# Optimization experiments

Measured on AMD Instinct MI355X. Metric: run time of the kernel, lower is better.

The kernel has to match this reference:

```python
import jax, jax.numpy as jnp
import numpy as np

B, N, D = 4, 4096, 64   # batch, num points, point-feature channels
K = 24                  # original_k_neighbors
GO = 128                # graph_out_channel = max(32, (D*2//8)*8)
MLP = [64, 128, 256]
HALF = MLP[-1] // 2     # graph_feature_mapping out channels
EPS = 1e-5

def leaky(x):
    return jnp.where(x > 0, x, 0.2 * x)

def bn(x, gamma, beta, axes):
    # training-mode batch norm (biased variance, like torch normalization); channel last
    m = jnp.mean(x, axes, keepdims=True)
    v = jnp.var(x, axes, keepdims=True)
    return (x - m) * jax.lax.rsqrt(v + EPS) * gamma + beta

def knn_idx(p, k):
    # p: [B,N,3] -> indices of k nearest neighbors (self excluded), [B,N,k]
    sq = jnp.sum(p * p, -1)
    dist = sq[:, :, None] + sq[:, None, :] - 2.0 * jnp.einsum('bnc,bmc->bnm', p, p)
    _, idx = jax.lax.top_k(-dist, k + 1)   # smallest k+1 distances
    return idx[:, :, 1:]

def setup_inputs():
    key = jax.random.key(0)
    ks = jax.random.split(key, 8)
    w = lambda i, s: jax.random.normal(ks[i], s, jnp.float32) * 0.05
    return {
        'xyz': jax.random.normal(ks[0], (B, 3, N), jnp.float32),
        'points': jax.random.normal(ks[1], (B, D, N), jnp.float32),
        'ec_w': w(2, (GO, 2 * D)),
        'ec_g': jnp.ones((GO,), jnp.float32), 'ec_b': jnp.zeros((GO,), jnp.float32),
        'gm_w': w(3, (HALF, GO)),
        'gm_g': jnp.ones((HALF,), jnp.float32), 'gm_b': jnp.zeros((HALF,), jnp.float32),
        'w0': w(4, (MLP[0], D + 3)), 'bias0': jnp.zeros((MLP[0],), jnp.float32),
        'g0': jnp.ones((MLP[0],), jnp.float32), 'be0': jnp.zeros((MLP[0],), jnp.float32),
        'w1': w(5, (MLP[1], MLP[0])), 'bias1': jnp.zeros((MLP[1],), jnp.float32),
        'g1': jnp.ones((MLP[1],), jnp.float32), 'be1': jnp.zeros((MLP[1],), jnp.float32),
        'w2': w(6, (MLP[2], MLP[1])), 'bias2': jnp.zeros((MLP[2],), jnp.float32),
        'g2': jnp.ones((MLP[2],), jnp.float32), 'be2': jnp.zeros((MLP[2],), jnp.float32),
        'fu_w': w(7, (MLP[2], MLP[2] + HALF)),
        'fu_g': jnp.ones((MLP[2],), jnp.float32), 'fu_b': jnp.zeros((MLP[2],), jnp.float32),
    }

def reference(xyz, points, ec_w, ec_g, ec_b, gm_w, gm_g, gm_b,
              w0, bias0, g0, be0, w1, bias1, g1, be1, w2, bias2, g2, be2,
              fu_w, fu_g, fu_b):
    xyz_t = jnp.transpose(xyz, (0, 2, 1))     # [B,N,3]
    pts_t = jnp.transpose(points, (0, 2, 1))  # [B,N,D]
    edges = knn_idx(xyz_t, K)                 # [B,N,K]
    # --- EdgeConv on original graph ---
    nb = jax.vmap(lambda f, e: f[e])(pts_t, edges)  # gather: [B,N,K,D]
    ctr = pts_t[:, :, None, :]
    ef = jnp.concatenate([jnp.broadcast_to(ctr, nb.shape), nb - ctr], -1)  # [B,N,K,2D]
    h = jnp.einsum('bnkc,oc->bnko', ef, ec_w)
    h = leaky(bn(h, ec_g, ec_b, (0, 1, 2)))
    gfeat = jnp.max(h, axis=2)                # max over neighbors -> [B,N,GO]
    # --- graph_feature_mapping ---
    gm = jnp.einsum('bnc,oc->bno', gfeat, gm_w)
    gm = leaky(bn(gm, gm_g, gm_b, (0, 1)))    # [B,N,HALF]
    # --- group_all PointNet MLP ---
    g = jnp.concatenate([xyz_t, pts_t], -1)   # [B,N,D+3]
    for wl, bl, gl, bel in ((w0, bias0, g0, be0), (w1, bias1, g1, be1), (w2, bias2, g2, be2)):
        g = jax.nn.relu(bn(jnp.einsum('bnc,oc->bno', g, wl) + bl, gl, bel, (0, 1)))
    point_feat = jnp.max(g, axis=1)           # [B, MLP[-1]]
    graph_glob = jnp.max(gm, axis=1)          # [B, HALF]
    # --- fusion ---
    fused = jnp.concatenate([point_feat, graph_glob], -1)
    f = jnp.einsum('bc,oc->bo', fused, fu_w)
    f = leaky(bn(f, fu_g, fu_b, (0,)))
    return f[:, :, None]                      # [B, MLP[-1], 1]
```

## Files before the change

### kernel.cpp

```cpp
#include <hip/hip_runtime.h>

#define NPTS 4096
#define QN   16384
#define KNN  24

static constexpr size_t OFF_EDGES = 0;
static constexpr size_t OFF_BIG   = 393216;
static constexpr size_t OFF_A     = OFF_BIG;
static constexpr size_t OFF_C     = OFF_BIG + 2097152;
static constexpr size_t OFF_M     = OFF_BIG + 4194304;
static constexpr size_t OFF_GM    = OFF_BIG + 6553600;
static constexpr size_t OFF_L0    = OFF_GM + 2097152;
static constexpr size_t OFF_L1    = OFF_L0 + 1048576;
static constexpr size_t OFF_L2    = OFF_L1 + 2097152;
static constexpr size_t ST_BASE   = OFF_L2 + 4194304;
static constexpr size_t ST_BN1    = ST_BASE;
static constexpr size_t ST_GM     = ST_BASE + 256;
static constexpr size_t ST_L0     = ST_BASE + 512;
static constexpr size_t ST_L1     = ST_BASE + 640;
static constexpr size_t ST_L2     = ST_BASE + 896;
static constexpr size_t OFF_PF    = ST_BASE + 1408;
static constexpr size_t OFF_GG    = ST_BASE + 2432;
static constexpr size_t ST_COUNT  = 2944;

__device__ inline unsigned fmap(float f) {
    unsigned u = __float_as_uint(f);
    return (u & 0x80000000u) ? ~u : (u | 0x80000000u);
}
__device__ inline float funmap(unsigned u) {
    unsigned v = (u & 0x80000000u) ? (u & 0x7fffffffu) : ~u;
    return __uint_as_float(v);
}

__device__ inline void xcd_map(int bid, int& b, int& chunk) {
    b = (bid & 7) >> 1;
    chunk = ((bid >> 3) << 1) | (bid & 1);
}

__global__ __launch_bounds__(256) void knn_kernel(const float* __restrict__ xyz,
                                                  int* __restrict__ edges) {
    __shared__ float4 cand[1024];
    __shared__ unsigned long long buf[4][128];
    int b = blockIdx.y;
    int wave = threadIdx.x >> 6;
    int lane = threadIdx.x & 63;
    int n = blockIdx.x * 4 + wave;
    const float* xb = xyz + (size_t)b * 3 * 4096;
    unsigned long long* wbuf = buf[wave];

    float xq = xb[n], yq = xb[4096 + n], zq = xb[8192 + n];
    float sqq = __fadd_rn(__fadd_rn(__fmul_rn(xq, xq), __fmul_rn(yq, yq)), __fmul_rn(zq, zq));

    unsigned T = 0xFFFFFFFFu;
    int count = 0;

    auto reduce = [&]() {
        unsigned long long ka = (lane < count) ? wbuf[lane] : ~0ull;
        int ra = 0;
        if (count > 64) {
            unsigned long long kb = (lane + 64 < count) ? wbuf[lane + 64] : ~0ull;
            int rb = 0;
            for (int j = 0; j < count; ++j) {
                unsigned long long kj = wbuf[j];
                ra += (kj < ka);
                rb += (kj < kb);
            }
            if (rb < 25) wbuf[rb] = kb;
        } else {
            for (int j = 0; j < count; ++j) {
                unsigned long long kj = wbuf[j];
                ra += (kj < ka);
            }
        }
        if (ra < 25) wbuf[ra] = ka;
        count = 25;
        T = (unsigned)(wbuf[24] >> 32);
    };

    for (int strip = 0; strip < 4; ++strip) {
        __syncthreads();
        for (int i = threadIdx.x; i < 1024; i += 256) {
            int j = strip * 1024 + i;
            float x = xb[j], y = xb[4096 + j], z = xb[8192 + j];
            float sq = __fadd_rn(__fadd_rn(__fmul_rn(x, x), __fmul_rn(y, y)), __fmul_rn(z, z));
            cand[i] = make_float4(x, y, z, sq);
        }
        __syncthreads();

        for (int t = 0; t < 16; ++t) {
            float4 cv = cand[t * 64 + lane];
            float dot = __fadd_rn(__fadd_rn(__fmul_rn(xq, cv.x), __fmul_rn(yq, cv.y)), __fmul_rn(zq, cv.z));
            float d = __fsub_rn(__fadd_rn(sqq, cv.w), __fmul_rn(2.0f, dot));
            unsigned du = fmap(d);
            bool surv = (du <= T);
            unsigned long long m = __ballot(surv);
            if (m) {
                if (surv) {
                    int ofs = __popcll(m & ((1ull << lane) - 1ull));
                    unsigned idx = (unsigned)(strip * 1024 + t * 64 + lane);
                    wbuf[count + ofs] = ((unsigned long long)du << 32) | idx;
                }
                count += (int)__popcll(m);
                if (count >= 64) reduce();
            }
        }
    }
    reduce();
    if (lane >= 1 && lane < 25)
        edges[((size_t)(b * 4096 + n)) * KNN + lane - 1] = (int)(unsigned)(wbuf[lane] & 0xFFFFFFFFull);
}

__global__ __launch_bounds__(256) void feat_kernel(const float* __restrict__ pts,
                                                   const float* __restrict__ ec_w,
                                                   float* __restrict__ afeat,
                                                   float* __restrict__ cfeat) {
    __shared__ float inl[64 * 65];
    __shared__ float wa[64 * 132];
    __shared__ float wc[64 * 132];
    int b, chunk;
    xcd_map(blockIdx.x, b, chunk);
    int n0 = chunk * 64;

    for (int idx = threadIdx.x; idx < 64 * 64; idx += 256) {
        int c = idx >> 6, p = idx & 63;
        inl[p * 65 + c] = pts[((size_t)(b * 64 + c) << 12) + n0 + p];
    }
    for (int idx = threadIdx.x; idx < 128 * 64; idx += 256) {
        int o = idx >> 6, cc = idx & 63;
        float w1 = ec_w[o * 128 + cc], w2 = ec_w[o * 128 + 64 + cc];
        wa[cc * 132 + o] = w1 - w2;
        wc[cc * 132 + o] = w2;
    }
    __syncthreads();

    int ng = threadIdx.x & 15, og = threadIdx.x >> 4;
    float acca[4][8], accc[4][8];
    #pragma unroll
    for (int r = 0; r < 4; ++r)
        #pragma unroll
        for (int i = 0; i < 8; ++i) { acca[r][i] = 0.f; accc[r][i] = 0.f; }

    for (int c = 0; c < 64; ++c) {
        float pv[4];
        #pragma unroll
        for (int r = 0; r < 4; ++r) pv[r] = inl[(ng * 4 + r) * 65 + c];
        const float* wra = &wa[c * 132 + og * 8];
        const float* wrc = &wc[c * 132 + og * 8];
        float4 a0 = *(const float4*)&wra[0];
        float4 a1 = *(const float4*)&wra[4];
        float4 c0 = *(const float4*)&wrc[0];
        float4 c1 = *(const float4*)&wrc[4];
        float wva[8] = {a0.x, a0.y, a0.z, a0.w, a1.x, a1.y, a1.z, a1.w};
        float wvc[8] = {c0.x, c0.y, c0.z, c0.w, c1.x, c1.y, c1.z, c1.w};
        #pragma unroll
        for (int r = 0; r < 4; ++r)
            #pragma unroll
            for (int i = 0; i < 8; ++i) {
                acca[r][i] = fmaf(pv[r], wva[i], acca[r][i]);
                accc[r][i] = fmaf(pv[r], wvc[i], accc[r][i]);
            }
    }
    __syncthreads();
    float* outl = wa;
    size_t base = (((size_t)b << 12) + n0) * 128;

    #pragma unroll
    for (int r = 0; r < 4; ++r)
        #pragma unroll
        for (int i = 0; i < 8; ++i)
            outl[(ng * 4 + r) * 132 + og * 8 + i] = acca[r][i];
    __syncthreads();
    for (int idx = threadIdx.x; idx < 64 * 128; idx += 256) {
        int p = idx >> 7, o = idx & 127;
        afeat[base + idx] = outl[p * 132 + o];
    }
    __syncthreads();
    #pragma unroll
    for (int r = 0; r < 4; ++r)
        #pragma unroll
        for (int i = 0; i < 8; ++i)
            outl[(ng * 4 + r) * 132 + og * 8 + i] = accc[r][i];
    __syncthreads();
    for (int idx = threadIdx.x; idx < 64 * 128; idx += 256) {
        int p = idx >> 7, o = idx & 127;
        cfeat[base + idx] = outl[p * 132 + o];
    }
}

__global__ __launch_bounds__(256) void gather_stats_kernel(const float* __restrict__ afeat,
                                                           const float* __restrict__ cfeat,
                                                           const int* __restrict__ edges,
                                                           float* __restrict__ M,
                                                           float* __restrict__ st) {
    __shared__ int eL[16 * KNN];
    __shared__ float red[8][132];
    int b, chunk;
    xcd_map(blockIdx.x, b, chunk);
    int q0 = b * 4096 + chunk * 16;
    for (int idx = threadIdx.x; idx < 16 * KNN; idx += 256) eL[idx] = edges[(size_t)q0 * KNN + idx];
    __syncthreads();

    int m = threadIdx.x & 31;
    int g = threadIdx.x >> 5;
    int bbase = b << 12;
    float s1[4] = {0.f, 0.f, 0.f, 0.f}, s2[4] = {0.f, 0.f, 0.f, 0.f};

    #pragma unroll
    for (int half = 0; half < 2; ++half) {
        int p = g + half * 8;
        int q = q0 + p;
        float mx0 = -__builtin_inff(), mx1 = mx0, mx2 = mx0, mx3 = mx0;
        float sv0 = 0.f, sv1 = 0.f, sv2 = 0.f, sv3 = 0.f;
        float qv0 = 0.f, qv1 = 0.f, qv2 = 0.f, qv3 = 0.f;
        #pragma unroll 8
        for (int k = 0; k < KNN; ++k) {
            int e = eL[p * KNN + k];
            float4 v = *(const float4*)&cfeat[((size_t)(bbase + e) << 7) + m * 4];
            mx0 = fmaxf(mx0, v.x); sv0 += v.x; qv0 = fmaf(v.x, v.x, qv0);
            mx1 = fmaxf(mx1, v.y); sv1 += v.y; qv1 = fmaf(v.y, v.y, qv1);
            mx2 = fmaxf(mx2, v.z); sv2 += v.z; qv2 = fmaf(v.z, v.z, qv2);
            mx3 = fmaxf(mx3, v.w); sv3 += v.w; qv3 = fmaf(v.w, v.w, qv3);
        }
        float4 a = *(const float4*)&afeat[((size_t)q << 7) + m * 4];
        float4 mo = make_float4(a.x + mx0, a.y + mx1, a.z + mx2, a.w + mx3);
        *(float4*)&M[((size_t)q << 7) + m * 4] = mo;
        s1[0] += fmaf(24.f, a.x, sv0); s2[0] += 24.f * a.x * a.x + 2.f * a.x * sv0 + qv0;
        s1[1] += fmaf(24.f, a.y, sv1); s2[1] += 24.f * a.y * a.y + 2.f * a.y * sv1 + qv1;
        s1[2] += fmaf(24.f, a.z, sv2); s2[2] += 24.f * a.z * a.z + 2.f * a.z * sv2 + qv2;
        s1[3] += fmaf(24.f, a.w, sv3); s2[3] += 24.f * a.w * a.w + 2.f * a.w * sv3 + qv3;
    }
    #pragma unroll
    for (int j = 0; j < 4; ++j) red[g][m * 4 + j] = s1[j];
    __syncthreads();
    if (threadIdx.x < 128) {
        float t = 0.f;
        #pragma unroll
        for (int gg = 0; gg < 8; ++gg) t += red[gg][threadIdx.x];
        atomicAdd(&st[threadIdx.x], t);
    }
    __syncthreads();
    #pragma unroll
    for (int j = 0; j < 4; ++j) red[g][m * 4 + j] = s2[j];
    __syncthreads();
    if (threadIdx.x < 128) {
        float t = 0.f;
        #pragma unroll
        for (int gg = 0; gg < 8; ++gg) t += red[gg][threadIdx.x];
        atomicAdd(&st[128 + threadIdx.x], t);
    }
}

template<int I, int O, int OSPLIT, int MODE>
__global__ __launch_bounds__(256) void layer_kernel(
    const float* __restrict__ inraw, const float* __restrict__ inst, float rcnt,
    const float* __restrict__ ing, const float* __restrict__ inbe,
    const float* __restrict__ W, const float* __restrict__ bias,
    const float* __restrict__ xyz, const float* __restrict__ pts,
    float* __restrict__ outraw, float* __restrict__ outst)
{
    constexpr int OH = O / OSPLIT;
    constexpr int IP = (I & 1) ? I : I + 1;
    constexpr int OP = OH + 4;
    constexpr int OW = OH / 16;
    __shared__ float inl[64 * IP];
    __shared__ float wl[64 * OP];
    __shared__ float ns[I], nb[I];

    int b, chunk;
    xcd_map(blockIdx.x, b, chunk);
    int q0 = b * 4096 + chunk * 64;
    int o0 = blockIdx.y * OH;

    if (MODE != 0) {
        if (threadIdx.x < I) {
            int c = threadIdx.x;
            float m = inst[c] * rcnt;
            float v = inst[I + c] * rcnt - m * m;
            float inv = 1.0f / sqrtf(v + 1e-5f);
            float sc = inv * ing[c];
            ns[c] = sc;
            nb[c] = inbe[c] - m * sc;
        }
        __syncthreads();
        const float* src = inraw + (size_t)q0 * I;
        for (int idx = threadIdx.x; idx < 64 * I; idx += 256) {
            int p = idx / I, c = idx - p * I;
            float v = fmaf(src[idx], ns[c], nb[c]);
            if (MODE == 1) v = fmaxf(v, 0.0f);
            else           v = (v > 0.0f) ? v : 0.2f * v;
            inl[p * IP + c] = v;
        }
    } else {
        int n0 = q0 & 4095;
        for (int idx = threadIdx.x; idx < 64 * I; idx += 256) {
            int c = idx >> 6, p = idx & 63;
            float v;
            if (c < 3) v = xyz[((size_t)(b * 3 + c) << 12) + n0 + p];
            else       v = pts[((size_t)(b * 64 + (c - 3)) << 12) + n0 + p];
            inl[p * IP + c] = v;
        }
    }

    int ng = threadIdx.x & 15, og = threadIdx.x >> 4;
    float acc[4][OW];
    #pragma unroll
    for (int r = 0; r < 4; ++r)
        #pragma unroll
        for (int i = 0; i < OW; ++i) acc[r][i] = 0.f;

    for (int ct = 0; ct < I; ct += 64) {
        int CT = (I - ct < 64) ? (I - ct) : 64;
        __syncthreads();
        for (int idx = threadIdx.x; idx < CT * OH; idx += 256) {
            int o = idx / CT, cc = idx - o * CT;
            wl[cc * OP + o] = W[(size_t)(o0 + o) * I + ct + cc];
        }
        __syncthreads();
        for (int cc = 0; cc < CT; ++cc) {
            int c = ct + cc;
            float pv[4];
            #pragma unroll
            for (int r = 0; r < 4; ++r) pv[r] = inl[(ng * 4 + r) * IP + c];
            const float* wr = &wl[cc * OP + og * OW];
            if constexpr ((OW & 3) == 0) {
                #pragma unroll
                for (int i4 = 0; i4 < OW / 4; ++i4) {
                    float4 wv = *(const float4*)&wr[i4 * 4];
                    #pragma unroll
                    for (int r = 0; r < 4; ++r) {
                        acc[r][i4 * 4 + 0] = fmaf(pv[r], wv.x, acc[r][i4 * 4 + 0]);
                        acc[r][i4 * 4 + 1] = fmaf(pv[r], wv.y, acc[r][i4 * 4 + 1]);
                        acc[r][i4 * 4 + 2] = fmaf(pv[r], wv.z, acc[r][i4 * 4 + 2]);
                        acc[r][i4 * 4 + 3] = fmaf(pv[r], wv.w, acc[r][i4 * 4 + 3]);
                    }
                }
            } else {
                float2 wv = *(const float2*)&wr[0];
                #pragma unroll
                for (int r = 0; r < 4; ++r) {
                    acc[r][0] = fmaf(pv[r], wv.x, acc[r][0]);
                    acc[r][1] = fmaf(pv[r], wv.y, acc[r][1]);
                }
            }
        }
    }

    if (bias != nullptr) {
        #pragma unroll
        for (int i = 0; i < OW; ++i) {
            float bv = bias[o0 + og * OW + i];
            #pragma unroll
            for (int r = 0; r < 4; ++r) acc[r][i] += bv;
        }
    }
    __syncthreads();
    #pragma unroll
    for (int r = 0; r < 4; ++r)
        #pragma unroll
        for (int i = 0; i < OW; ++i)
            wl[(ng * 4 + r) * OP + og * OW + i] = acc[r][i];
    __syncthreads();

    for (int idx = threadIdx.x; idx < 64 * OH; idx += 256) {
        int p = idx / OH, o = idx - p * OH;
        outraw[(size_t)(q0 + p) * O + o0 + o] = wl[p * OP + o];
    }
    if (threadIdx.x < OH) {
        int o = threadIdx.x;
        float s1 = 0.f, s2 = 0.f;
        #pragma unroll 8
        for (int p = 0; p < 64; ++p) {
            float v = wl[p * OP + o];
            s1 += v;
            s2 = fmaf(v, v, s2);
        }
        atomicAdd(&outst[o0 + o], s1);
        atomicAdd(&outst[O + o0 + o], s2);
    }
}

__global__ __launch_bounds__(256) void fin2_kernel(const float* __restrict__ gm_raw,
                                                   const float* __restrict__ stGM,
                                                   const float* __restrict__ gm_g,
                                                   const float* __restrict__ gm_b,
                                                   const float* __restrict__ l2_raw,
                                                   const float* __restrict__ stL2,
                                                   const float* __restrict__ g2,
                                                   const float* __restrict__ be2,
                                                   unsigned* __restrict__ gg,
                                                   unsigned* __restrict__ pf) {
    const float rcnt = 1.0f / 16384.0f;
    int b = blockIdx.y & 3;
    int p0 = blockIdx.x * 128;
    if (blockIdx.y < 4) {
        int o = threadIdx.x & 127, rep = threadIdx.x >> 7;
        float m = stGM[o] * rcnt;
        float v = stGM[128 + o] * rcnt - m * m;
        float sc = gm_g[o] / sqrtf(v + 1e-5f);
        float sh = gm_b[o] - m * sc;
        float mx = -__builtin_inff();
        for (int p = rep; p < 128; p += 2) {
            float x = fmaf(gm_raw[(size_t)(b * 4096 + p0 + p) * 128 + o], sc, sh);
            x = (x > 0.0f) ? x : 0.2f * x;
            mx = fmaxf(mx, x);
        }
        atomicMax(&gg[b * 128 + o], fmap(mx));
    } else {
        int o = threadIdx.x;
        float m = stL2[o] * rcnt;
        float v = stL2[256 + o] * rcnt - m * m;
        float sc = g2[o] / sqrtf(v + 1e-5f);
        float sh = be2[o] - m * sc;
        float mx = -__builtin_inff();
        for (int p = 0; p < 128; ++p) {
            float x = fmaf(l2_raw[(size_t)(b * 4096 + p0 + p) * 256 + o], sc, sh);
            x = fmaxf(x, 0.0f);
            mx = fmaxf(mx, x);
        }
        atomicMax(&pf[b * 256 + o], fmap(mx));
    }
}

__global__ __launch_bounds__(256) void final_kernel(const unsigned* __restrict__ pf,
                                                    const unsigned* __restrict__ gg,
                                                    const float* __restrict__ fu_w,
                                                    const float* __restrict__ fu_g,
                                                    const float* __restrict__ fu_b,
                                                    float* __restrict__ out) {
    __shared__ float fl[4 * 384];
    for (int idx = threadIdx.x; idx < 4 * 384; idx += 256) {
        int b = idx / 384, c = idx - b * 384;
        unsigned u = (c < 256) ? pf[b * 256 + c] : gg[b * 128 + (c - 256)];
        fl[idx] = funmap(u);
    }
    __syncthreads();
    int o = threadIdx.x;
    float f[4];
    #pragma unroll
    for (int b = 0; b < 4; ++b) {
        float acc = 0.f;
        for (int c = 0; c < 384; ++c) acc = fmaf(fl[b * 384 + c], fu_w[(size_t)o * 384 + c], acc);
        f[b] = acc;
    }
    float m = 0.25f * (f[0] + f[1] + f[2] + f[3]);
    float var = 0.f;
    #pragma unroll
    for (int b = 0; b < 4; ++b) { float t = f[b] - m; var = fmaf(t, t, var); }
    var *= 0.25f;
    float inv = 1.0f / sqrtf(var + 1e-5f);
    float gv = fu_g[o], bv = fu_b[o];
    #pragma unroll
    for (int b = 0; b < 4; ++b) {
        float x = (f[b] - m) * inv * gv + bv;
        x = (x > 0.0f) ? x : 0.2f * x;
        out[b * 256 + o] = x;
    }
}

extern "C" void kernel_launch(void* const* d_in, const int* in_sizes, int n_in,
                              void* d_out, int out_size, void* d_ws, size_t ws_size,
                              hipStream_t stream) {
    const float* xyz   = (const float*)d_in[0];
    const float* pts   = (const float*)d_in[1];
    const float* ec_w  = (const float*)d_in[2];
    const float* ec_g  = (const float*)d_in[3];
    const float* ec_b  = (const float*)d_in[4];
    const float* gm_w  = (const float*)d_in[5];
    const float* gm_g  = (const float*)d_in[6];
    const float* gm_b  = (const float*)d_in[7];
    const float* w0    = (const float*)d_in[8];
    const float* bias0 = (const float*)d_in[9];
    const float* g0    = (const float*)d_in[10];
    const float* be0   = (const float*)d_in[11];
    const float* w1    = (const float*)d_in[12];
    const float* bias1 = (const float*)d_in[13];
    const float* g1    = (const float*)d_in[14];
    const float* be1   = (const float*)d_in[15];
    const float* w2    = (const float*)d_in[16];
    const float* bias2 = (const float*)d_in[17];
    const float* g2    = (const float*)d_in[18];
    const float* be2   = (const float*)d_in[19];
    const float* fu_w  = (const float*)d_in[20];
    const float* fu_g  = (const float*)d_in[21];
    const float* fu_b  = (const float*)d_in[22];

    float* ws = (float*)d_ws;
    float* out = (float*)d_out;

    hipMemsetAsync(ws + ST_BASE, 0, ST_COUNT * sizeof(float), stream);

    knn_kernel<<<dim3(NPTS / 4, 4), 256, 0, stream>>>(xyz, (int*)(ws + OFF_EDGES));

    feat_kernel<<<256, 256, 0, stream>>>(pts, ec_w, ws + OFF_A, ws + OFF_C);
    gather_stats_kernel<<<QN / 16, 256, 0, stream>>>(ws + OFF_A, ws + OFF_C, (int*)(ws + OFF_EDGES),
                                                     ws + OFF_M, ws + ST_BN1);

    layer_kernel<128, 128, 2, 2><<<dim3(256, 2), 256, 0, stream>>>(
        ws + OFF_M, ws + ST_BN1, 1.0f / 393216.0f, ec_g, ec_b,
        gm_w, nullptr, nullptr, nullptr, ws + OFF_GM, ws + ST_GM);

    layer_kernel<67, 64, 2, 0><<<dim3(256, 2), 256, 0, stream>>>(
        nullptr, nullptr, 0.f, nullptr, nullptr,
        w0, bias0, xyz, pts, ws + OFF_L0, ws + ST_L0);
    layer_kernel<64, 128, 2, 1><<<dim3(256, 2), 256, 0, stream>>>(
        ws + OFF_L0, ws + ST_L0, 1.0f / 16384.0f, g0, be0,
        w1, bias1, nullptr, nullptr, ws + OFF_L1, ws + ST_L1);
    layer_kernel<128, 256, 4, 1><<<dim3(256, 4), 256, 0, stream>>>(
        ws + OFF_L1, ws + ST_L1, 1.0f / 16384.0f, g1, be1,
        w2, bias2, nullptr, nullptr, ws + OFF_L2, ws + ST_L2);

    fin2_kernel<<<dim3(32, 8), 256, 0, stream>>>(
        ws + OFF_GM, ws + ST_GM, gm_g, gm_b,
        ws + OFF_L2, ws + ST_L2, g2, be2,
        (unsigned*)(ws + OFF_GG), (unsigned*)(ws + OFF_PF));

    final_kernel<<<1, 256, 0, stream>>>((unsigned*)(ws + OFF_PF), (unsigned*)(ws + OFF_GG),
                                        fu_w, fu_g, fu_b, out);
}
```

Baseline: 396.3 us.

## Merge pipeline stages into five multi-role kernels with last-block fusion tail

```diff
diff --git a/kernel.cpp b/kernel.cpp
--- a/kernel.cpp
+++ b/kernel.cpp
@@ -21,7 +21,8 @@
 static constexpr size_t ST_L2     = ST_BASE + 896;
 static constexpr size_t OFF_PF    = ST_BASE + 1408;
 static constexpr size_t OFF_GG    = ST_BASE + 2432;
-static constexpr size_t ST_COUNT  = 2944;
+static constexpr size_t ST_TICKET = ST_BASE + 2944;
+static constexpr int    ST_COUNT  = 2945;
 
 __device__ inline unsigned fmap(float f) {
     unsigned u = __float_as_uint(f);
@@ -32,244 +33,26 @@
     return __uint_as_float(v);
 }
 
-__device__ inline void xcd_map(int bid, int& b, int& chunk) {
-    b = (bid & 7) >> 1;
-    chunk = ((bid >> 3) << 1) | (bid & 1);
-}
-
-__global__ __launch_bounds__(256) void knn_kernel(const float* __restrict__ xyz,
-                                                  int* __restrict__ edges) {
-    __shared__ float4 cand[1024];
-    __shared__ unsigned long long buf[4][128];
-    int b = blockIdx.y;
-    int wave = threadIdx.x >> 6;
-    int lane = threadIdx.x & 63;
-    int n = blockIdx.x * 4 + wave;
-    const float* xb = xyz + (size_t)b * 3 * 4096;
-    unsigned long long* wbuf = buf[wave];
-
-    float xq = xb[n], yq = xb[4096 + n], zq = xb[8192 + n];
-    float sqq = __fadd_rn(__fadd_rn(__fmul_rn(xq, xq), __fmul_rn(yq, yq)), __fmul_rn(zq, zq));
-
-    unsigned T = 0xFFFFFFFFu;
-    int count = 0;
-
-    auto reduce = [&]() {
-        unsigned long long ka = (lane < count) ? wbuf[lane] : ~0ull;
-        int ra = 0;
-        if (count > 64) {
-            unsigned long long kb = (lane + 64 < count) ? wbuf[lane + 64] : ~0ull;
-            int rb = 0;
-            for (int j = 0; j < count; ++j) {
-                unsigned long long kj = wbuf[j];
-                ra += (kj < ka);
-                rb += (kj < kb);
-            }
-            if (rb < 25) wbuf[rb] = kb;
-        } else {
-            for (int j = 0; j < count; ++j) {
-                unsigned long long kj = wbuf[j];
-                ra += (kj < ka);
-            }
-        }
-        if (ra < 25) wbuf[ra] = ka;
-        count = 25;
-        T = (unsigned)(wbuf[24] >> 32);
-    };
-
-    for (int strip = 0; strip < 4; ++strip) {
-        __syncthreads();
-        for (int i = threadIdx.x; i < 1024; i += 256) {
-            int j = strip * 1024 + i;
-            float x = xb[j], y = xb[4096 + j], z = xb[8192 + j];
-            float sq = __fadd_rn(__fadd_rn(__fmul_rn(x, x), __fmul_rn(y, y)), __fmul_rn(z, z));
-            cand[i] = make_float4(x, y, z, sq);
-        }
-        __syncthreads();
-
-        for (int t = 0; t < 16; ++t) {
-            float4 cv = cand[t * 64 + lane];
-            float dot = __fadd_rn(__fadd_rn(__fmul_rn(xq, cv.x), __fmul_rn(yq, cv.y)), __fmul_rn(zq, cv.z));
-            float d = __fsub_rn(__fadd_rn(sqq, cv.w), __fmul_rn(2.0f, dot));
-            unsigned du = fmap(d);
-            bool surv = (du <= T);
-            unsigned long long m = __ballot(surv);
-            if (m) {
-                if (surv) {
-                    int ofs = __popcll(m & ((1ull << lane) - 1ull));
-                    unsigned idx = (unsigned)(strip * 1024 + t * 64 + lane);
-                    wbuf[count + ofs] = ((unsigned long long)du << 32) | idx;
-                }
-                count += (int)__popcll(m);
-                if (count >= 64) reduce();
-            }
-        }
-    }
-    reduce();
-    if (lane >= 1 && lane < 25)
-        edges[((size_t)(b * 4096 + n)) * KNN + lane - 1] = (int)(unsigned)(wbuf[lane] & 0xFFFFFFFFull);
-}
-
-__global__ __launch_bounds__(256) void feat_kernel(const float* __restrict__ pts,
-                                                   const float* __restrict__ ec_w,
-                                                   float* __restrict__ afeat,
-                                                   float* __restrict__ cfeat) {
-    __shared__ float inl[64 * 65];
-    __shared__ float wa[64 * 132];
-    __shared__ float wc[64 * 132];
-    int b, chunk;
-    xcd_map(blockIdx.x, b, chunk);
-    int n0 = chunk * 64;
-
-    for (int idx = threadIdx.x; idx < 64 * 64; idx += 256) {
-        int c = idx >> 6, p = idx & 63;
-        inl[p * 65 + c] = pts[((size_t)(b * 64 + c) << 12) + n0 + p];
-    }
-    for (int idx = threadIdx.x; idx < 128 * 64; idx += 256) {
-        int o = idx >> 6, cc = idx & 63;
-        float w1 = ec_w[o * 128 + cc], w2 = ec_w[o * 128 + 64 + cc];
-        wa[cc * 132 + o] = w1 - w2;
-        wc[cc * 132 + o] = w2;
-    }
-    __syncthreads();
-
-    int ng = threadIdx.x & 15, og = threadIdx.x >> 4;
-    float acca[4][8], accc[4][8];
-    #pragma unroll
-    for (int r = 0; r < 4; ++r)
-        #pragma unroll
-        for (int i = 0; i < 8; ++i) { acca[r][i] = 0.f; accc[r][i] = 0.f; }
-
-    for (int c = 0; c < 64; ++c) {
-        float pv[4];
-        #pragma unroll
-        for (int r = 0; r < 4; ++r) pv[r] = inl[(ng * 4 + r) * 65 + c];
-        const float* wra = &wa[c * 132 + og * 8];
-        const float* wrc = &wc[c * 132 + og * 8];
-        float4 a0 = *(const float4*)&wra[0];
-        float4 a1 = *(const float4*)&wra[4];
-        float4 c0 = *(const float4*)&wrc[0];
-        float4 c1 = *(const float4*)&wrc[4];
-        float wva[8] = {a0.x, a0.y, a0.z, a0.w, a1.x, a1.y, a1.z, a1.w};
-        float wvc[8] = {c0.x, c0.y, c0.z, c0.w, c1.x, c1.y, c1.z, c1.w};
-        #pragma unroll
-        for (int r = 0; r < 4; ++r)
-            #pragma unroll
-            for (int i = 0; i < 8; ++i) {
-                acca[r][i] = fmaf(pv[r], wva[i], acca[r][i]);
-                accc[r][i] = fmaf(pv[r], wvc[i], accc[r][i]);
-            }
-    }
-    __syncthreads();
-    float* outl = wa;
-    size_t base = (((size_t)b << 12) + n0) * 128;
-
-    #pragma unroll
-    for (int r = 0; r < 4; ++r)
-        #pragma unroll
-        for (int i = 0; i < 8; ++i)
-            outl[(ng * 4 + r) * 132 + og * 8 + i] = acca[r][i];
-    __syncthreads();
-    for (int idx = threadIdx.x; idx < 64 * 128; idx += 256) {
-        int p = idx >> 7, o = idx & 127;
-        afeat[base + idx] = outl[p * 132 + o];
-    }
-    __syncthreads();
-    #pragma unroll
-    for (int r = 0; r < 4; ++r)
-        #pragma unroll
-        for (int i = 0; i < 8; ++i)
-            outl[(ng * 4 + r) * 132 + og * 8 + i] = accc[r][i];
-    __syncthreads();
-    for (int idx = threadIdx.x; idx < 64 * 128; idx += 256) {
-        int p = idx >> 7, o = idx & 127;
-        cfeat[base + idx] = outl[p * 132 + o];
-    }
-}
-
-__global__ __launch_bounds__(256) void gather_stats_kernel(const float* __restrict__ afeat,
-                                                           const float* __restrict__ cfeat,
-                                                           const int* __restrict__ edges,
-                                                           float* __restrict__ M,
-                                                           float* __restrict__ st) {
-    __shared__ int eL[16 * KNN];
-    __shared__ float red[8][132];
-    int b, chunk;
-    xcd_map(blockIdx.x, b, chunk);
-    int q0 = b * 4096 + chunk * 16;
-    for (int idx = threadIdx.x; idx < 16 * KNN; idx += 256) eL[idx] = edges[(size_t)q0 * KNN + idx];
-    __syncthreads();
-
-    int m = threadIdx.x & 31;
-    int g = threadIdx.x >> 5;
-    int bbase = b << 12;
-    float s1[4] = {0.f, 0.f, 0.f, 0.f}, s2[4] = {0.f, 0.f, 0.f, 0.f};
-
-    #pragma unroll
-    for (int half = 0; half < 2; ++half) {
-        int p = g + half * 8;
-        int q = q0 + p;
-        float mx0 = -__builtin_inff(), mx1 = mx0, mx2 = mx0, mx3 = mx0;
-        float sv0 = 0.f, sv1 = 0.f, sv2 = 0.f, sv3 = 0.f;
-        float qv0 = 0.f, qv1 = 0.f, qv2 = 0.f, qv3 = 0.f;
-        #pragma unroll 8
-        for (int k = 0; k < KNN; ++k) {
-            int e = eL[p * KNN + k];
-            float4 v = *(const float4*)&cfeat[((size_t)(bbase + e) << 7) + m * 4];
-            mx0 = fmaxf(mx0, v.x); sv0 += v.x; qv0 = fmaf(v.x, v.x, qv0);
-            mx1 = fmaxf(mx1, v.y); sv1 += v.y; qv1 = fmaf(v.y, v.y, qv1);
-            mx2 = fmaxf(mx2, v.z); sv2 += v.z; qv2 = fmaf(v.z, v.z, qv2);
-            mx3 = fmaxf(mx3, v.w); sv3 += v.w; qv3 = fmaf(v.w, v.w, qv3);
-        }
-        float4 a = *(const float4*)&afeat[((size_t)q << 7) + m * 4];
-        float4 mo = make_float4(a.x + mx0, a.y + mx1, a.z + mx2, a.w + mx3);
-        *(float4*)&M[((size_t)q << 7) + m * 4] = mo;
-        s1[0] += fmaf(24.f, a.x, sv0); s2[0] += 24.f * a.x * a.x + 2.f * a.x * sv0 + qv0;
-        s1[1] += fmaf(24.f, a.y, sv1); s2[1] += 24.f * a.y * a.y + 2.f * a.y * sv1 + qv1;
-        s1[2] += fmaf(24.f, a.z, sv2); s2[2] += 24.f * a.z * a.z + 2.f * a.z * sv2 + qv2;
-        s1[3] += fmaf(24.f, a.w, sv3); s2[3] += 24.f * a.w * a.w + 2.f * a.w * sv3 + qv3;
-    }
-    #pragma unroll
-    for (int j = 0; j < 4; ++j) red[g][m * 4 + j] = s1[j];
-    __syncthreads();
-    if (threadIdx.x < 128) {
-        float t = 0.f;
-        #pragma unroll
-        for (int gg = 0; gg < 8; ++gg) t += red[gg][threadIdx.x];
-        atomicAdd(&st[threadIdx.x], t);
-    }
-    __syncthreads();
-    #pragma unroll
-    for (int j = 0; j < 4; ++j) red[g][m * 4 + j] = s2[j];
-    __syncthreads();
-    if (threadIdx.x < 128) {
-        float t = 0.f;
-        #pragma unroll
-        for (int gg = 0; gg < 8; ++gg) t += red[gg][threadIdx.x];
-        atomicAdd(&st[128 + threadIdx.x], t);
-    }
-}
-
-template<int I, int O, int OSPLIT, int MODE>
-__global__ __launch_bounds__(256) void layer_kernel(
+__device__ inline void xcd_decode(int v, int& b, int& t) {
+    b = (v & 7) >> 1;
+    t = ((v >> 3) << 1) | (v & 1);
+}
+
+template<int I, int O, int OH, int MODE, bool HASBIAS>
+__device__ void layer_part(unsigned char* smem, int b, int chunk, int o0,
     const float* __restrict__ inraw, const float* __restrict__ inst, float rcnt,
     const float* __restrict__ ing, const float* __restrict__ inbe,
     const float* __restrict__ W, const float* __restrict__ bias,
     const float* __restrict__ xyz, const float* __restrict__ pts,
     float* __restrict__ outraw, float* __restrict__ outst)
 {
-    constexpr int OH = O / OSPLIT;
-    constexpr int IP = (I & 1) ? I : I + 1;
+    constexpr int OW = OH / 16;
     constexpr int OP = OH + 4;
-    constexpr int OW = OH / 16;
-    __shared__ float inl[64 * IP];
-    __shared__ float wl[64 * OP];
-    __shared__ float ns[I], nb[I];
-
-    int b, chunk;
-    xcd_map(blockIdx.x, b, chunk);
+    float* ns  = (float*)smem;
+    float* nb  = ns + I;
+    float* inl = nb + I;
+    float* wl  = inl + 64 * 65;
     int q0 = b * 4096 + chunk * 64;
-    int o0 = blockIdx.y * OH;
 
     if (MODE != 0) {
         if (threadIdx.x < I) {
@@ -281,24 +64,6 @@
             ns[c] = sc;
             nb[c] = inbe[c] - m * sc;
         }
-        __syncthreads();
-        const float* src = inraw + (size_t)q0 * I;
-        for (int idx = threadIdx.x; idx < 64 * I; idx += 256) {
-            int p = idx / I, c = idx - p * I;
-            float v = fmaf(src[idx], ns[c], nb[c]);
-            if (MODE == 1) v = fmaxf(v, 0.0f);
-            else           v = (v > 0.0f) ? v : 0.2f * v;
-            inl[p * IP + c] = v;
-        }
-    } else {
-        int n0 = q0 & 4095;
-        for (int idx = threadIdx.x; idx < 64 * I; idx += 256) {
-            int c = idx >> 6, p = idx & 63;
-            float v;
-            if (c < 3) v = xyz[((size_t)(b * 3 + c) << 12) + n0 + p];
-            else       v = pts[((size_t)(b * 64 + (c - 3)) << 12) + n0 + p];
-            inl[p * IP + c] = v;
-        }
     }
 
     int ng = threadIdx.x & 15, og = threadIdx.x >> 4;
@@ -311,31 +76,53 @@
     for (int ct = 0; ct < I; ct += 64) {
         int CT = (I - ct < 64) ? (I - ct) : 64;
         __syncthreads();
-        for (int idx = threadIdx.x; idx < CT * OH; idx += 256) {
-            int o = idx / CT, cc = idx - o * CT;
-            wl[cc * OP + o] = W[(size_t)(o0 + o) * I + ct + cc];
+        if (MODE == 0) {
+            for (int idx = threadIdx.x; idx < CT * 64; idx += 256) {
+                int c = idx >> 6, p = idx & 63;
+                int ch = ct + c;
+                float v = (ch < 3) ? xyz[((size_t)(b * 3 + ch) << 12) + chunk * 64 + p]
+                                   : pts[((size_t)(b * 64 + ch - 3) << 12) + chunk * 64 + p];
+                inl[p * 65 + c] = v;
+            }
+        } else {
+            const float* src = inraw + (size_t)q0 * I + ct;
+            for (int idx = threadIdx.x; idx < 64 * 64; idx += 256) {
+                int p = idx >> 6, c = idx & 63;
+                if (c < CT) {
+                    float v = fmaf(src[(size_t)p * I + c], ns[ct + c], nb[ct + c]);
+                    v = (MODE == 1) ? fmaxf(v, 0.0f) : ((v > 0.0f) ? v : 0.2f * v);
+                    inl[p * 65 + c] = v;
+                }
+            }
+        }
+        if (CT == 64) {
+            for (int idx = threadIdx.x; idx < 64 * OH; idx += 256) {
+                int o = idx >> 6, cc = idx & 63;
+                wl[cc * OP + o] = W[(size_t)(o0 + o) * I + ct + cc];
+            }
+        } else {
+            for (int idx = threadIdx.x; idx < CT * OH; idx += 256) {
+                int o = idx / CT, cc = idx - o * CT;
+                wl[cc * OP + o] = W[(size_t)(o0 + o) * I + ct + cc];
+            }
         }
         __syncthreads();
         for (int cc = 0; cc < CT; ++cc) {
-            int c = ct + cc;
             float pv[4];
             #pragma unroll
-            for (int r = 0; r < 4; ++r) pv[r] = inl[(ng * 4 + r) * IP + c];
+            for (int r = 0; r < 4; ++r) pv[r] = inl[(ng * 4 + r) * 65 + cc];
             const float* wr = &wl[cc * OP + og * OW];
-            if constexpr ((OW & 3) == 0) {
+            if constexpr (OW == 4) {
+                float4 wv = *(const float4*)wr;
                 #pragma unroll
-                for (int i4 = 0; i4 < OW / 4; ++i4) {
-                    float4 wv = *(const float4*)&wr[i4 * 4];
-                    #pragma unroll
-                    for (int r = 0; r < 4; ++r) {
-                        acc[r][i4 * 4 + 0] = fmaf(pv[r], wv.x, acc[r][i4 * 4 + 0]);
-                        acc[r][i4 * 4 + 1] = fmaf(pv[r], wv.y, acc[r][i4 * 4 + 1]);
-                        acc[r][i4 * 4 + 2] = fmaf(pv[r], wv.z, acc[r][i4 * 4 + 2]);
-                        acc[r][i4 * 4 + 3] = fmaf(pv[r], wv.w, acc[r][i4 * 4 + 3]);
-                    }
+                for (int r = 0; r < 4; ++r) {
+                    acc[r][0] = fmaf(pv[r], wv.x, acc[r][0]);
+                    acc[r][1] = fmaf(pv[r], wv.y, acc[r][1]);
+                    acc[r][2] = fmaf(pv[r], wv.z, acc[r][2]);
+                    acc[r][3] = fmaf(pv[r], wv.w, acc[r][3]);
                 }
             } else {
-                float2 wv = *(const float2*)&wr[0];
+                float2 wv = *(const float2*)wr;
                 #pragma unroll
                 for (int r = 0; r < 4; ++r) {
                     acc[r][0] = fmaf(pv[r], wv.x, acc[r][0]);
@@ -345,7 +132,7 @@
         }
     }
 
-    if (bias != nullptr) {
+    if (HASBIAS) {
         #pragma unroll
         for (int i = 0; i < OW; ++i) {
             float bv = bias[o0 + og * OW + i];
@@ -379,20 +166,294 @@
     }
 }
 
-__global__ __launch_bounds__(256) void fin2_kernel(const float* __restrict__ gm_raw,
-                                                   const float* __restrict__ stGM,
-                                                   const float* __restrict__ gm_g,
-                                                   const float* __restrict__ gm_b,
-                                                   const float* __restrict__ l2_raw,
-                                                   const float* __restrict__ stL2,
-                                                   const float* __restrict__ g2,
-                                                   const float* __restrict__ be2,
-                                                   unsigned* __restrict__ gg,
-                                                   unsigned* __restrict__ pf) {
+__global__ __launch_bounds__(256) void kA(const float* __restrict__ xyz,
+                                          const float* __restrict__ pts,
+                                          const float* __restrict__ ec_w,
+                                          int* __restrict__ edges,
+                                          float* __restrict__ afeat,
+                                          float* __restrict__ cfeat,
+                                          float* __restrict__ stz) {
+    __shared__ __align__(16) unsigned char smem[25856];
+    int u = blockIdx.x;
+    if (u < 4096) {
+        float4* cand = (float4*)smem;
+        unsigned long long* bufall = (unsigned long long*)(smem + 16384);
+        int b = u >> 10;
+        int wave = threadIdx.x >> 6, lane = threadIdx.x & 63;
+        int n = ((u & 1023) << 2) + wave;
+        const float* xb = xyz + (size_t)b * 3 * 4096;
+        unsigned long long* wbuf = bufall + wave * 128;
+
+        float xq = xb[n], yq = xb[4096 + n], zq = xb[8192 + n];
+        float sqq = __fadd_rn(__fadd_rn(__fmul_rn(xq, xq), __fmul_rn(yq, yq)), __fmul_rn(zq, zq));
+
+        unsigned T = 0xFFFFFFFFu;
+        int count = 0;
+
+        auto reduce = [&]() {
+            unsigned long long ka = (lane < count) ? wbuf[lane] : ~0ull;
+            int ra = 0;
+            if (count > 64) {
+                unsigned long long kb = (lane + 64 < count) ? wbuf[lane + 64] : ~0ull;
+                int rb = 0;
+                for (int j = 0; j < count; ++j) {
+                    unsigned long long kj = wbuf[j];
+                    ra += (kj < ka);
+                    rb += (kj < kb);
+                }
+                if (rb < 25) wbuf[rb] = kb;
+            } else {
+                for (int j = 0; j < count; ++j) {
+                    unsigned long long kj = wbuf[j];
+                    ra += (kj < ka);
+                }
+            }
+            if (ra < 25) wbuf[ra] = ka;
+            count = 25;
+            T = (unsigned)(wbuf[24] >> 32);
+        };
+
+        for (int strip = 0; strip < 4; ++strip) {
+            __syncthreads();
+            for (int i = threadIdx.x; i < 1024; i += 256) {
+                int j = strip * 1024 + i;
+                float x = xb[j], y = xb[4096 + j], z = xb[8192 + j];
+                float sq = __fadd_rn(__fadd_rn(__fmul_rn(x, x), __fmul_rn(y, y)), __fmul_rn(z, z));
+                cand[i] = make_float4(x, y, z, sq);
+            }
+            __syncthreads();
+            for (int t = 0; t < 16; ++t) {
+                float4 cv = cand[t * 64 + lane];
+                float dot = __fadd_rn(__fadd_rn(__fmul_rn(xq, cv.x), __fmul_rn(yq, cv.y)), __fmul_rn(zq, cv.z));
+                float d = __fsub_rn(__fadd_rn(sqq, cv.w), __fmul_rn(2.0f, dot));
+                unsigned du = fmap(d);
+                bool surv = (du <= T);
+                unsigned long long m = __ballot(surv);
+                if (m) {
+                    if (surv) {
+                        int ofs = __popcll(m & ((1ull << lane) - 1ull));
+                        unsigned idx = (unsigned)(strip * 1024 + t * 64 + lane);
+                        wbuf[count + ofs] = ((unsigned long long)du << 32) | idx;
+                    }
+                    count += (int)__popcll(m);
+                    if (count >= 64) reduce();
+                }
+            }
+        }
+        reduce();
+        if (lane >= 1 && lane < 25)
+            edges[((size_t)(b * 4096 + n)) * KNN + lane - 1] = (int)(unsigned)(wbuf[lane] & 0xFFFFFFFFull);
+    } else if (u < 6144) {
+        int v = u - 4096;
+        int b, t;
+        xcd_decode(v, b, t);
+        int nchunk = t & 63, sub = t >> 6;
+        int which = sub >> 2;
+        int o0 = (sub & 3) * 32;
+        int n0 = nchunk * 64;
+
+        float* inl = (float*)smem;
+        float* wl  = (float*)(smem + 16640);
+        const float* pb = pts + (size_t)b * 64 * 4096;
+
+        for (int idx = threadIdx.x; idx < 64 * 64; idx += 256) {
+            int c = idx >> 6, p = idx & 63;
+            inl[p * 65 + c] = pb[(size_t)c * 4096 + n0 + p];
+        }
+        for (int idx = threadIdx.x; idx < 64 * 32; idx += 256) {
+            int cc = idx & 63, o = idx >> 6;
+            float w2v = ec_w[(o0 + o) * 128 + 64 + cc];
+            wl[cc * 36 + o] = which ? w2v : (ec_w[(o0 + o) * 128 + cc] - w2v);
+        }
+        __syncthreads();
+
+        int ng = threadIdx.x & 15, og = threadIdx.x >> 4;
+        float acc[4][2] = {{0.f, 0.f}, {0.f, 0.f}, {0.f, 0.f}, {0.f, 0.f}};
+        for (int cc = 0; cc < 64; ++cc) {
+            float pv[4];
+            #pragma unroll
+            for (int r = 0; r < 4; ++r) pv[r] = inl[(ng * 4 + r) * 65 + cc];
+            float2 wv = *(const float2*)&wl[cc * 36 + og * 2];
+            #pragma unroll
+            for (int r = 0; r < 4; ++r) {
+                acc[r][0] = fmaf(pv[r], wv.x, acc[r][0]);
+                acc[r][1] = fmaf(pv[r], wv.y, acc[r][1]);
+            }
+        }
+        __syncthreads();
+        #pragma unroll
+        for (int r = 0; r < 4; ++r) {
+            wl[(ng * 4 + r) * 36 + og * 2 + 0] = acc[r][0];
+            wl[(ng * 4 + r) * 36 + og * 2 + 1] = acc[r][1];
+        }
+        __syncthreads();
+        float* dst = (which ? cfeat : afeat) + ((size_t)(b * 4096 + n0)) * 128 + o0;
+        for (int idx = threadIdx.x; idx < 64 * 32; idx += 256) {
+            int p = idx >> 5, o = idx & 31;
+            dst[(size_t)p * 128 + o] = wl[p * 36 + o];
+        }
+    } else {
+        for (int i = threadIdx.x; i < ST_COUNT; i += 256) stz[i] = 0.f;
+    }
+}
+
+__global__ __launch_bounds__(256) void kB(const float* __restrict__ afeat,
+                                          const float* __restrict__ cfeat,
+                                          const int* __restrict__ edges,
+                                          float* __restrict__ M,
+                                          float* __restrict__ stBN1,
+                                          const float* __restrict__ xyz,
+                                          const float* __restrict__ pts,
+                                          const float* __restrict__ w0,
+                                          const float* __restrict__ bias0,
+                                          float* __restrict__ l0raw,
+                                          float* __restrict__ stL0) {
+    __shared__ __align__(16) unsigned char smem[26368];
+    int u = blockIdx.x;
+    if (u < 1024) {
+        int* eL = (int*)smem;
+        float* red = (float*)(smem + 1536);
+        int b, chunk;
+        xcd_decode(u, b, chunk);
+        int q0 = b * 4096 + chunk * 16;
+        for (int idx = threadIdx.x; idx < 16 * KNN; idx += 256) eL[idx] = edges[(size_t)q0 * KNN + idx];
+        __syncthreads();
+
+        int m = threadIdx.x & 31;
+        int g = threadIdx.x >> 5;
+        int bbase = b << 12;
+        float s1[4] = {0.f, 0.f, 0.f, 0.f}, s2[4] = {0.f, 0.f, 0.f, 0.f};
+
+        #pragma unroll
+        for (int half = 0; half < 2; ++half) {
+            int p = g + half * 8;
+            int q = q0 + p;
+            float mx0 = -__builtin_inff(), mx1 = mx0, mx2 = mx0, mx3 = mx0;
+            float sv0 = 0.f, sv1 = 0.f, sv2 = 0.f, sv3 = 0.f;
+            float qv0 = 0.f, qv1 = 0.f, qv2 = 0.f, qv3 = 0.f;
+            #pragma unroll 8
+            for (int k = 0; k < KNN; ++k) {
+                int e = eL[p * KNN + k];
+                float4 v = *(const float4*)&cfeat[((size_t)(bbase + e) << 7) + m * 4];
+                mx0 = fmaxf(mx0, v.x); sv0 += v.x; qv0 = fmaf(v.x, v.x, qv0);
+                mx1 = fmaxf(mx1, v.y); sv1 += v.y; qv1 = fmaf(v.y, v.y, qv1);
+                mx2 = fmaxf(mx2, v.z); sv2 += v.z; qv2 = fmaf(v.z, v.z, qv2);
+                mx3 = fmaxf(mx3, v.w); sv3 += v.w; qv3 = fmaf(v.w, v.w, qv3);
+            }
+            float4 a = *(const float4*)&afeat[((size_t)q << 7) + m * 4];
+            float4 mo = make_float4(a.x + mx0, a.y + mx1, a.z + mx2, a.w + mx3);
+            *(float4*)&M[((size_t)q << 7) + m * 4] = mo;
+            s1[0] += fmaf(24.f, a.x, sv0); s2[0] += 24.f * a.x * a.x + 2.f * a.x * sv0 + qv0;
+            s1[1] += fmaf(24.f, a.y, sv1); s2[1] += 24.f * a.y * a.y + 2.f * a.y * sv1 + qv1;
+            s1[2] += fmaf(24.f, a.z, sv2); s2[2] += 24.f * a.z * a.z + 2.f * a.z * sv2 + qv2;
+            s1[3] += fmaf(24.f, a.w, sv3); s2[3] += 24.f * a.w * a.w + 2.f * a.w * sv3 + qv3;
+        }
+        #pragma unroll
+        for (int j = 0; j < 4; ++j) red[g * 132 + m * 4 + j] = s1[j];
+        __syncthreads();
+        if (threadIdx.x < 128) {
+            float t = 0.f;
+            #pragma unroll
+            for (int gg = 0; gg < 8; ++gg) t += red[gg * 132 + threadIdx.x];
+            atomicAdd(&stBN1[threadIdx.x], t);
+        }
+        __syncthreads();
+        #pragma unroll
+        for (int j = 0; j < 4; ++j) red[g * 132 + m * 4 + j] = s2[j];
+        __syncthreads();
+        if (threadIdx.x < 128) {
+            float t = 0.f;
+            #pragma unroll
+            for (int gg = 0; gg < 8; ++gg) t += red[gg * 132 + threadIdx.x];
+            atomicAdd(&stBN1[128 + threadIdx.x], t);
+        }
+    } else {
+        int v = u - 1024;
+        int b, t;
+        xcd_decode(v, b, t);
+        int chunk = t & 63, y = t >> 6;
+        layer_part<67, 64, 32, 0, true>(smem, b, chunk, y * 32,
+            nullptr, nullptr, 0.f, nullptr, nullptr,
+            w0, bias0, xyz, pts, l0raw, stL0);
+    }
+}
+
+__global__ __launch_bounds__(256) void kC(const float* __restrict__ M,
+                                          const float* __restrict__ stBN1,
+                                          const float* __restrict__ ec_g,
+                                          const float* __restrict__ ec_b,
+                                          const float* __restrict__ gm_w,
+                                          float* __restrict__ gmraw,
+                                          float* __restrict__ stGM,
+                                          const float* __restrict__ l0raw,
+                                          const float* __restrict__ stL0,
+                                          const float* __restrict__ g0,
+                                          const float* __restrict__ be0,
+                                          const float* __restrict__ w1,
+                                          const float* __restrict__ bias1,
+                                          float* __restrict__ l1raw,
+                                          float* __restrict__ stL1) {
+    __shared__ __align__(16) unsigned char smem[35072];
+    int u = blockIdx.x;
+    if (u < 512) {
+        int b, t;
+        xcd_decode(u, b, t);
+        int chunk = t & 63, y = t >> 6;
+        layer_part<128, 128, 64, 2, false>(smem, b, chunk, y * 64,
+            M, stBN1, 1.0f / 393216.0f, ec_g, ec_b,
+            gm_w, nullptr, nullptr, nullptr, gmraw, stGM);
+    } else {
+        int v = u - 512;
+        int b, t;
+        xcd_decode(v, b, t);
+        int chunk = t & 63, y = t >> 6;
+        layer_part<64, 128, 64, 1, true>(smem, b, chunk, y * 64,
+            l0raw, stL0, 1.0f / 16384.0f, g0, be0,
+            w1, bias1, nullptr, nullptr, l1raw, stL1);
+    }
+}
+
+__global__ __launch_bounds__(256) void kD(const float* __restrict__ l1raw,
+                                          const float* __restrict__ stL1,
+                                          const float* __restrict__ g1,
+                                          const float* __restrict__ be1,
+                                          const float* __restrict__ w2,
+                                          const float* __restrict__ bias2,
+                                          float* __restrict__ l2raw,
+                                          float* __restrict__ stL2) {
+    __shared__ __align__(16) unsigned char smem[35072];
+    int u = blockIdx.x;
+    int b, t;
+    xcd_decode(u, b, t);
+    int chunk = t & 63, y = t >> 6;
+    layer_part<128, 256, 64, 1, true>(smem, b, chunk, y * 64,
+        l1raw, stL1, 1.0f / 16384.0f, g1, be1,
+        w2, bias2, nullptr, nullptr, l2raw, stL2);
+}
+
+__global__ __launch_bounds__(256) void kE(const float* __restrict__ gm_raw,
+                                          const float* __restrict__ stGM,
+                                          const float* __restrict__ gm_g,
+                                          const float* __restrict__ gm_b,
+                                          const float* __restrict__ l2_raw,
+                                          const float* __restrict__ stL2,
+                                          const float* __restrict__ g2,
+                                          const float* __restrict__ be2,
+                                          unsigned* __restrict__ gg,
+                                          unsigned* __restrict__ pf,
+                                          unsigned* __restrict__ ticket,
+                                          const float* __restrict__ fu_w,
+                                          const float* __restrict__ fu_g,
+                                          const float* __restrict__ fu_b,
+                                          float* __restrict__ out) {
+    __shared__ __align__(16) unsigned char smem[6400];
+    __shared__ int isLast;
     const float rcnt = 1.0f / 16384.0f;
-    int b = blockIdx.y & 3;
-    int p0 = blockIdx.x * 128;
-    if (blockIdx.y < 4) {
+    int u = blockIdx.x;
+    int y = u >> 5, x = u & 31;
+    int b = y & 3;
+    int p0 = x * 128;
+    if (y < 4) {
         int o = threadIdx.x & 127, rep = threadIdx.x >> 7;
         float m = stGM[o] * rcnt;
         float v = stGM[128 + o] * rcnt - m * m;
@@ -400,9 +461,9 @@
         float sh = gm_b[o] - m * sc;
         float mx = -__builtin_inff();
         for (int p = rep; p < 128; p += 2) {
-            float x = fmaf(gm_raw[(size_t)(b * 4096 + p0 + p) * 128 + o], sc, sh);
-            x = (x > 0.0f) ? x : 0.2f * x;
-            mx = fmaxf(mx, x);
+            float xx = fmaf(gm_raw[(size_t)(b * 4096 + p0 + p) * 128 + o], sc, sh);
+            xx = (xx > 0.0f) ? xx : 0.2f * xx;
+            mx = fmaxf(mx, xx);
         }
         atomicMax(&gg[b * 128 + o], fmap(mx));
     } else {
@@ -413,47 +474,49 @@
         float sh = be2[o] - m * sc;
         float mx = -__builtin_inff();
         for (int p = 0; p < 128; ++p) {
-            float x = fmaf(l2_raw[(size_t)(b * 4096 + p0 + p) * 256 + o], sc, sh);
-            x = fmaxf(x, 0.0f);
-            mx = fmaxf(mx, x);
+            float xx = fmaf(l2_raw[(size_t)(b * 4096 + p0 + p) * 256 + o], sc, sh);
+            xx = fmaxf(xx, 0.0f);
+            mx = fmaxf(mx, xx);
         }
         atomicMax(&pf[b * 256 + o], fmap(mx));
     }
-}
-
-__global__ __launch_bounds__(256) void final_kernel(const unsigned* __restrict__ pf,
-                                                    const unsigned* __restrict__ gg,
-                                                    const float* __restrict__ fu_w,
-                                                    const float* __restrict__ fu_g,
-                                                    const float* __restrict__ fu_b,
-                                                    float* __restrict__ out) {
-    __shared__ float fl[4 * 384];
-    for (int idx = threadIdx.x; idx < 4 * 384; idx += 256) {
-        int b = idx / 384, c = idx - b * 384;
-        unsigned u = (c < 256) ? pf[b * 256 + c] : gg[b * 128 + (c - 256)];
-        fl[idx] = funmap(u);
-    }
     __syncthreads();
-    int o = threadIdx.x;
-    float f[4];
-    #pragma unroll
-    for (int b = 0; b < 4; ++b) {
-        float acc = 0.f;
-        for (int c = 0; c < 384; ++c) acc = fmaf(fl[b * 384 + c], fu_w[(size_t)o * 384 + c], acc);
-        f[b] = acc;
-    }
-    float m = 0.25f * (f[0] + f[1] + f[2] + f[3]);
-    float var = 0.f;
-    #pragma unroll
-    for (int b = 0; b < 4; ++b) { float t = f[b] - m; var = fmaf(t, t, var); }
-    var *= 0.25f;
-    float inv = 1.0f / sqrtf(var + 1e-5f);
-    float gv = fu_g[o], bv = fu_b[o];
-    #pragma unroll
-    for (int b = 0; b < 4; ++b) {
-        float x = (f[b] - m) * inv * gv + bv;
-        x = (x > 0.0f) ? x : 0.2f * x;
-        out[b * 256 + o] = x;
+    if (threadIdx.x == 0) {
+        __threadfence();
+        unsigned old = atomicAdd(ticket, 1u);
+        isLast = (old == 255u);
+    }
+    __syncthreads();
+    if (isLast) {
+        float* fl = (float*)smem;
+        for (int idx = threadIdx.x; idx < 4 * 384; idx += 256) {
+            int bb = idx / 384, c = idx - bb * 384;
+            unsigned uu = (c < 256) ? atomicMax(&pf[bb * 256 + c], 0u)
+                                    : atomicMax(&gg[bb * 128 + (c - 256)], 0u);
+            fl[idx] = funmap(uu);
+        }
+        __syncthreads();
+        int o = threadIdx.x;
+        float f[4];
+        #pragma unroll
+        for (int bb = 0; bb < 4; ++bb) {
+            float acc = 0.f;
+            for (int c = 0; c < 384; ++c) acc = fmaf(fl[bb * 384 + c], fu_w[(size_t)o * 384 + c], acc);
+            f[bb] = acc;
+        }
+        float m = 0.25f * (f[0] + f[1] + f[2] + f[3]);
+        float var = 0.f;
+        #pragma unroll
+        for (int bb = 0; bb < 4; ++bb) { float tt = f[bb] - m; var = fmaf(tt, tt, var); }
+        var *= 0.25f;
+        float inv = 1.0f / sqrtf(var + 1e-5f);
+        float gv = fu_g[o], bv = fu_b[o];
+        #pragma unroll
+        for (int bb = 0; bb < 4; ++bb) {
+            float xx = (f[bb] - m) * inv * gv + bv;
+            xx = (xx > 0.0f) ? xx : 0.2f * xx;
+            out[bb * 256 + o] = xx;
+        }
     }
 }
 
@@ -487,33 +550,20 @@
     float* ws = (float*)d_ws;
     float* out = (float*)d_out;
 
-    hipMemsetAsync(ws + ST_BASE, 0, ST_COUNT * sizeof(float), stream);
-
-    knn_kernel<<<dim3(NPTS / 4, 4), 256, 0, stream>>>(xyz, (int*)(ws + OFF_EDGES));
-
-    feat_kernel<<<256, 256, 0, stream>>>(pts, ec_w, ws + OFF_A, ws + OFF_C);
-    gather_stats_kernel<<<QN / 16, 256, 0, stream>>>(ws + OFF_A, ws + OFF_C, (int*)(ws + OFF_EDGES),
-                                                     ws + OFF_M, ws + ST_BN1);
-
-    layer_kernel<128, 128, 2, 2><<<dim3(256, 2), 256, 0, stream>>>(
-        ws + OFF_M, ws + ST_BN1, 1.0f / 393216.0f, ec_g, ec_b,
-        gm_w, nullptr, nullptr, nullptr, ws + OFF_GM, ws + ST_GM);
-
-    layer_kernel<67, 64, 2, 0><<<dim3(256, 2), 256, 0, stream>>>(
-        nullptr, nullptr, 0.f, nullptr, nullptr,
-        w0, bias0, xyz, pts, ws + OFF_L0, ws + ST_L0);
-    layer_kernel<64, 128, 2, 1><<<dim3(256, 2), 256, 0, stream>>>(
-        ws + OFF_L0, ws + ST_L0, 1.0f / 16384.0f, g0, be0,
-        w1, bias1, nullptr, nullptr, ws + OFF_L1, ws + ST_L1);
-    layer_kernel<128, 256, 4, 1><<<dim3(256, 4), 256, 0, stream>>>(
-        ws + OFF_L1, ws + ST_L1, 1.0f / 16384.0f, g1, be1,
-        w2, bias2, nullptr, nullptr, ws + OFF_L2, ws + ST_L2);
-
-    fin2_kernel<<<dim3(32, 8), 256, 0, stream>>>(
-        ws + OFF_GM, ws + ST_GM, gm_g, gm_b,
-        ws + OFF_L2, ws + ST_L2, g2, be2,
-        (unsigned*)(ws + OFF_GG), (unsigned*)(ws + OFF_PF));
-
-    final_kernel<<<1, 256, 0, stream>>>((unsigned*)(ws + OFF_PF), (unsigned*)(ws + OFF_GG),
-                                        fu_w, fu_g, fu_b, out);
-}
+    kA<<<6145, 256, 0, stream>>>(xyz, pts, ec_w, (int*)(ws + OFF_EDGES),
+                                 ws + OFF_A, ws + OFF_C, ws + ST_BASE);
+    kB<<<1536, 256, 0, stream>>>(ws + OFF_A, ws + OFF_C, (int*)(ws + OFF_EDGES),
+                                 ws + OFF_M, ws + ST_BN1,
+                                 xyz, pts, w0, bias0, ws + OFF_L0, ws + ST_L0);
+    kC<<<1024, 256, 0, stream>>>(ws + OFF_M, ws + ST_BN1, ec_g, ec_b, gm_w,
+                                 ws + OFF_GM, ws + ST_GM,
+                                 ws + OFF_L0, ws + ST_L0, g0, be0, w1, bias1,
+                                 ws + OFF_L1, ws + ST_L1);
+    kD<<<1024, 256, 0, stream>>>(ws + OFF_L1, ws + ST_L1, g1, be1, w2, bias2,
+                                 ws + OFF_L2, ws + ST_L2);
+    kE<<<256, 256, 0, stream>>>(ws + OFF_GM, ws + ST_GM, gm_g, gm_b,
+                                ws + OFF_L2, ws + ST_L2, g2, be2,
+                                (unsigned*)(ws + OFF_GG), (unsigned*)(ws + OFF_PF),
+                                (unsigned*)(ws + ST_TICKET),
+                                fu_w, fu_g, fu_b, out);
+}
```

After: 360.4 us. -9.1%, faster.
